# Optimization experiments

Hardware: AMD Instinct MI355X
Metric: run time of the kernel (lower is better)

Reference implementation:

```python
import jax, jax.numpy as jnp
import numpy as np

B, V, E = 32, 2048, 12288
IMG_F = 512
GCN_DIMS = [(3 + IMG_F, 512), (512, 512), (512, 512), (512, 512), (512, 64), (64, 3)]
FC_DIMS = [(V * 3, 1024), (1024, 1024), (1024, V * 3)]


def setup_inputs() -> dict:
    key = jax.random.key(0)
    ks = jax.random.split(key, 3 + len(GCN_DIMS) + len(FC_DIMS))
    inp = {}
    inp["vertices"] = jax.random.normal(ks[0], (B, V, 3), dtype=jnp.float32)
    inp["img_features"] = jax.random.normal(ks[1], (B, IMG_F), dtype=jnp.float32)
    inp["edge_index"] = jax.random.randint(ks[2], (2, E), 0, V, dtype=jnp.int32)
    for i, (fi, fo) in enumerate(GCN_DIMS):
        inp[f"W{i+1}"] = (jax.random.normal(ks[3 + i], (fi, fo), dtype=jnp.float32) / np.sqrt(fi)).astype(jnp.float32)
        inp[f"b{i+1}"] = jnp.zeros((fo,), dtype=jnp.float32)
    for i, (fi, fo) in enumerate(FC_DIMS):
        inp[f"fcW{i+1}"] = (jax.random.normal(ks[3 + len(GCN_DIMS) + i], (fi, fo), dtype=jnp.float32) / np.sqrt(fi)).astype(jnp.float32)
        inp[f"fcb{i+1}"] = jnp.zeros((fo,), dtype=jnp.float32)
    return inp


def _gcn_norm(edge_index):
    # PyG GCNConv: add self-loops, symmetric normalization 1/sqrt(d_i d_j).
    loop = jnp.arange(V, dtype=edge_index.dtype)
    src = jnp.concatenate([edge_index[0], loop])
    dst = jnp.concatenate([edge_index[1], loop])
    deg = jax.ops.segment_sum(jnp.ones_like(dst, dtype=jnp.float32), dst, num_segments=V)
    dinv = jax.lax.rsqrt(deg)  # deg >= 1 due to self-loops
    norm = dinv[src] * dinv[dst]  # [E+V]
    return src, dst, norm


def _gcn_layer(x, W, b, src, dst, norm):
    # x: [B, V, Fin] -> [B, V, Fout]; transform then gather/scatter aggregate.
    h = jnp.einsum("bvi,io->bvo", x, W)
    msg = h[:, src, :] * norm[None, :, None]          # gather over edges
    agg = jax.vmap(lambda m: jax.ops.segment_sum(m, dst, num_segments=V))(msg)
    return agg + b


def reference(vertices, img_features, edge_index,
              W1, b1, W2, b2, W3, b3, W4, b4, W5, b5, W6, b6,
              fcW1, fcb1, fcW2, fcb2, fcW3, fcb3):
    src, dst, norm = _gcn_norm(edge_index)
    # concat vertex coords with broadcast image feature: [B, V, 3+512]
    x = jnp.concatenate([vertices, jnp.broadcast_to(img_features[:, None, :], (B, V, IMG_F))], axis=2)
    x = _gcn_layer(x, W1, b1, src, dst, norm)
    x = _gcn_layer(x, W2, b2, src, dst, norm)
    x = jax.nn.relu(x)
    x = _gcn_layer(x, W3, b3, src, dst, norm)
    x = _gcn_layer(x, W4, b4, src, dst, norm)
    x = jax.nn.relu(x)
    x = _gcn_layer(x, W5, b5, src, dst, norm)
    x = _gcn_layer(x, W6, b6, src, dst, norm)
    x = jax.nn.relu(x)
    x = x.reshape(B, V * 3)
    h = x @ fcW1 + fcb1
    h = h @ fcW2 + fcb2
    h = jnp.tanh(h @ fcW3 + fcb3)
    deformations = h.reshape(B, V, 3) * 0.1
    return vertices + deformations
```

## Files before the change

### kernel.cpp

```cpp
#include <hip/hip_runtime.h>
#include <stdint.h>
#include <math.h>

#define B_ 32
#define V_ 2048
#define E_ 12288
#define M_ (B_*V_)

typedef __bf16 bf16x8 __attribute__((ext_vector_type(8)));
typedef float f32x4 __attribute__((ext_vector_type(4)));

__device__ __forceinline__ float bf2f(unsigned short u){
  union { unsigned int i; float f; } v; v.i = ((unsigned int)u) << 16; return v.f;
}
__device__ __forceinline__ unsigned short f2bf(float f){
  union { float f; unsigned int i; } v; v.f = f;
  unsigned int r = (v.i + 0x7fffu + ((v.i >> 16) & 1u)) >> 16;
  return (unsigned short)r;
}
__device__ __forceinline__ void gload16(const unsigned short* g, unsigned short* l){
  __builtin_amdgcn_global_load_lds(
      (const __attribute__((address_space(1))) void*)g,
      (__attribute__((address_space(3))) void*)l, 16, 0, 0);
}

__global__ __launch_bounds__(1024) void k_pre0(
    const int* __restrict__ ei, int* __restrict__ rowptr_g, int* __restrict__ cols_g,
    float* __restrict__ vals_g, float* __restrict__ selfw_g,
    float* __restrict__ wsum_g, float* __restrict__ w2_g,
    const float* __restrict__ W3, const float* __restrict__ W4,
    const float* __restrict__ img, const float* __restrict__ W1,
    const float* __restrict__ b3, const float* __restrict__ W5,
    const float* __restrict__ W6, const float* __restrict__ b5,
    unsigned short* __restrict__ W3B, unsigned short* __restrict__ W4T,
    float* __restrict__ partB,
    float* __restrict__ C34, float* __restrict__ W56, float* __restrict__ C56){
  __shared__ int   sdeg[V_];
  __shared__ int   srp[V_ + 1];
  __shared__ int   sfill[V_];
  __shared__ float sdinv[V_];
  __shared__ float swsum[V_];
  __shared__ float sw2[V_];
  __shared__ int   swt[16];
  __shared__ __align__(16) float tile[4][32][33];
  if (blockIdx.x == 0){
    const int t = threadIdx.x;
    sdeg[2*t] = 0; sdeg[2*t+1] = 0; sfill[2*t] = 0; sfill[2*t+1] = 0;
    __syncthreads();
    #pragma unroll
    for (int e = t; e < E_; e += 1024) atomicAdd(&sdeg[ei[E_ + e]], 1);
    __syncthreads();
    int c0 = sdeg[2*t], c1 = sdeg[2*t+1];
    int s2 = c0 + c1;
    int lane = t & 63, wid = t >> 6;
    int pre = s2;
    #pragma unroll
    for (int off = 1; off < 64; off <<= 1){
      int u = __shfl_up(pre, off);
      if (lane >= off) pre += u;
    }
    if (lane == 63) swt[wid] = pre;
    __syncthreads();
    if (t == 0){
      int run = 0;
      #pragma unroll
      for (int i = 0; i < 16; i++){ int x = swt[i]; swt[i] = run; run += x; }
      srp[V_] = run;
    }
    __syncthreads();
    int base = swt[wid] + (pre - s2);
    srp[2*t] = base; srp[2*t+1] = base + c0;
    #pragma unroll
    for (int v = t; v < V_; v += 1024){
      float d = (float)(sdeg[v] + 1);
      float di = rsqrtf(d);
      sdinv[v] = di;
      swsum[v] = di * di;
    }
    __syncthreads();
    #pragma unroll
    for (int e = t; e < E_; e += 1024){
      int s = ei[e], d = ei[E_ + e];
      int pos = srp[d] + atomicAdd(&sfill[d], 1);
      float val = sdinv[s] * sdinv[d];
      cols_g[pos] = s;
      vals_g[pos] = val;
      atomicAdd(&swsum[d], val);
    }
    __syncthreads();
    #pragma unroll
    for (int v = t; v < V_; v += 1024)
      sw2[v] = (sdinv[v] * sdinv[v]) * swsum[v];
    __syncthreads();
    #pragma unroll
    for (int e = t; e < E_; e += 1024){
      int s = ei[e], d = ei[E_ + e];
      atomicAdd(&sw2[d], sdinv[s] * sdinv[d] * swsum[s]);
    }
    __syncthreads();
    #pragma unroll
    for (int v = t; v < V_; v += 1024){
      rowptr_g[v] = srp[v];
      selfw_g[v]  = sdinv[v] * sdinv[v];
      wsum_g[v]   = swsum[v];
      w2_g[v]     = sw2[v];
    }
    if (t == 0) rowptr_g[V_] = srp[V_];
  } else {
    int u = blockIdx.x - 1;
    int t10 = threadIdx.x;
    int sub = (u << 2) + (t10 >> 8);
    int t = t10 & 255;
    int ti = t10 >> 8;
    if (sub < 256){
      int tr0 = (sub >> 4) << 5, tc0 = (sub & 15) << 5;
      int r = t >> 5, c = t & 31;
      #pragma unroll
      for (int i = 0; i < 4; i++)
        tile[ti][r + 8*i][c] = W4[(size_t)(tr0 + r + 8*i) * 512 + tc0 + c];
      __syncthreads();
      #pragma unroll
      for (int i = 0; i < 4; i++)
        W4T[(size_t)(tc0 + r + 8*i) * 512 + tr0 + c] = f2bf(tile[ti][c][r + 8*i]);
    } else if (sub < 256 + 1024){
      int id = (sub - 256) * 256 + t;
      W3B[id] = f2bf(W3[id]);
    } else if (sub < 1344){
      int g = sub - 1280;
      int kc = g >> 1, nh = g & 1;
      int k0 = kc * 16;
      float* xs = &tile[ti][0][0];
      for (int i = t; i < 512; i += 256)
        xs[i] = img[(size_t)(i >> 4) * 512 + k0 + (i & 15)];
      __syncthreads();
      const float* W = W1 + 3 * 512;
      int n = (nh << 8) + t;
      float acc[32] = {};
      #pragma unroll
      for (int kg = 0; kg < 4; kg++){
        const float* wp = W + (size_t)(k0 + kg * 4) * 512 + n;
        float w0 = wp[0], w1 = wp[512], w2 = wp[1024], w3 = wp[1536];
        #pragma unroll
        for (int r = 0; r < 32; r++){
          f32x4 xv = *(const f32x4*)&xs[r * 16 + kg * 4];
          acc[r] += xv[0]*w0 + xv[1]*w1 + xv[2]*w2 + xv[3]*w3;
        }
      }
      float* p = partB + (size_t)kc * 16384 + n;
      #pragma unroll
      for (int r = 0; r < 32; r++) p[(size_t)r * 512] = acc[r];
    } else if (sub < 1346){
      int id = (sub - 1344) * 256 + t;
      float a0=0,a1=0,a2=0,a3=0;
      for (int k = 0; k < 512; k += 4){
        a0 += b3[k]   * W4[(size_t)k * 512 + id];
        a1 += b3[k+1] * W4[(size_t)(k+1) * 512 + id];
        a2 += b3[k+2] * W4[(size_t)(k+2) * 512 + id];
        a3 += b3[k+3] * W4[(size_t)(k+3) * 512 + id];
      }
      C34[id] = a0+a1+a2+a3;
    } else if (sub < 1352){
      int i = (sub - 1346) * 256 + t;
      int k5 = i / 3, j = i % 3;
      float a = 0.f;
      #pragma unroll 4
      for (int uu = 0; uu < 64; uu++) a += W5[k5 * 64 + uu] * W6[uu * 3 + j];
      W56[i] = a;
    } else if (sub == 1352){
      if (t < 3){
        float a = 0.f;
        #pragma unroll 4
        for (int uu = 0; uu < 64; uu++) a += b5[uu] * W6[uu * 3 + t];
        C56[t] = a;
      }
    }
  }
}

__global__ __launch_bounds__(256) void k_preC(
    const float* __restrict__ b1, const float* __restrict__ W1,
    const float* __restrict__ W2,
    const float* __restrict__ partIn, float* __restrict__ partOut){
  __shared__ __align__(16) float xs[36 * 16];
  int g = blockIdx.x;
  int kc = g >> 1, k0 = kc * 16;
  int t = threadIdx.x;
  int n = ((g & 1) << 8) + t;
  for (int i = t; i < 576; i += 256){
    int r = i >> 4, kk = i & 15;
    float val;
    if (r == 0)      val = b1[k0 + kk];
    else if (r < 4)  val = W1[(size_t)(r - 1) * 512 + k0 + kk];
    else {
      float a = 0.f;
      #pragma unroll
      for (int s = 0; s < 32; s++)
        a += partIn[(size_t)s * 16384 + (size_t)(r - 4) * 512 + k0 + kk];
      val = a;
    }
    xs[i] = val;
  }
  __syncthreads();
  float acc[36] = {};
  #pragma unroll
  for (int kg = 0; kg < 4; kg++){
    const float* wp = W2 + (size_t)(k0 + kg * 4) * 512 + n;
    float w0 = wp[0], w1 = wp[512], w2 = wp[1024], w3 = wp[1536];
    #pragma unroll
    for (int r = 0; r < 36; r++){
      f32x4 xv = *(const f32x4*)&xs[r * 16 + kg * 4];
      acc[r] += xv[0]*w0 + xv[1]*w1 + xv[2]*w2 + xv[3]*w3;
    }
  }
  float* p = partOut + (size_t)kc * 18432 + n;
  #pragma unroll
  for (int r = 0; r < 36; r++) p[(size_t)r * 512] = acc[r];
}

__global__ __launch_bounds__(256) void k_preD(
    const float* __restrict__ partB, float* __restrict__ P){
  int id = blockIdx.x * 256 + threadIdx.x;
  float a = 0.f;
  #pragma unroll
  for (int s = 0; s < 32; s++) a += partB[(size_t)s * 18432 + id];
  P[id] = a;
}

__global__ __launch_bounds__(256) void k_va2a(
    const float* __restrict__ in, const int* __restrict__ rowptr,
    const int* __restrict__ cols, const float* __restrict__ vals,
    const float* __restrict__ selfw, float* __restrict__ yout){
  __shared__ float xs[V_ * 3];
  int b = blockIdx.y, t = threadIdx.x;
  const float* ib = in + (size_t)b * V_ * 3;
  for (int i = t; i < V_ * 3; i += 256) xs[i] = ib[i];
  __syncthreads();
  int v = blockIdx.x * 256 + t;
  float sw = selfw[v];
  float a0 = sw * xs[v*3], a1 = sw * xs[v*3+1], a2 = sw * xs[v*3+2];
  int re = rowptr[v + 1];
  for (int e = rowptr[v]; e < re; e++){
    int s = cols[e]; float vv = vals[e];
    a0 += vv * xs[s*3]; a1 += vv * xs[s*3+1]; a2 += vv * xs[s*3+2];
  }
  float* o = yout + (size_t)b * V_ * 3 + v * 3;
  o[0] = a0; o[1] = a1; o[2] = a2;
}

__global__ __launch_bounds__(256) void k_va2b(
    const float* __restrict__ yin, const int* __restrict__ rowptr,
    const int* __restrict__ cols, const float* __restrict__ vals,
    const float* __restrict__ selfw, float* __restrict__ outv){
  __shared__ float xs[V_ * 3];
  int b = blockIdx.y, t = threadIdx.x;
  const float* ib = yin + (size_t)b * V_ * 3;
  for (int i = t; i < V_ * 3; i += 256) xs[i] = ib[i];
  __syncthreads();
  int v = blockIdx.x * 256 + t;
  float sw = selfw[v];
  float a0 = sw * xs[v*3], a1 = sw * xs[v*3+1], a2 = sw * xs[v*3+2];
  int re = rowptr[v + 1];
  for (int e = rowptr[v]; e < re; e++){
    int s = cols[e]; float vv = vals[e];
    a0 += vv * xs[s*3]; a1 += vv * xs[s*3+1]; a2 += vv * xs[s*3+2];
  }
  float* o = outv + ((size_t)v * 32 + b) * 3;
  o[0] = a0; o[1] = a1; o[2] = a2;
}

__global__ __launch_bounds__(1024) void k_x2(
    const float* __restrict__ va2v, const float* __restrict__ P,
    const float* __restrict__ wsum, const float* __restrict__ w2s,
    const float* __restrict__ b2,
    unsigned short* __restrict__ Y){
  int v = (blockIdx.x << 2) + (threadIdx.x >> 8);
  int batch = (blockIdx.y << 2) + ((threadIdx.x >> 6) & 3);
  int f8 = (threadIdx.x & 63) * 8;
  const float* va = va2v + ((size_t)v * 32 + batch) * 3;
  float x0 = va[0], x1 = va[1], x2 = va[2];
  float w2v = w2s[v], wsv = wsum[v];
  float tt[8];
  #pragma unroll
  for (int h = 0; h < 2; h++){
    f32x4 wv0 = *(const f32x4*)&P[512  + f8 + 4*h];
    f32x4 wv1 = *(const f32x4*)&P[1024 + f8 + 4*h];
    f32x4 wv2 = *(const f32x4*)&P[1536 + f8 + 4*h];
    f32x4 ccv = *(const f32x4*)&P[f8 + 4*h];
    f32x4 bbv = *(const f32x4*)&b2[f8 + 4*h];
    f32x4 iiv = *(const f32x4*)&P[2048 + (size_t)batch * 512 + f8 + 4*h];
    #pragma unroll
    for (int j = 0; j < 4; j++){
      float tv = x0*wv0[j] + x1*wv1[j] + x2*wv2[j] + w2v*iiv[j] + wsv*ccv[j] + bbv[j];
      tt[4*h + j] = fmaxf(tv, 0.f);
    }
  }
  unsigned int o[4];
  #pragma unroll
  for (int i = 0; i < 4; i++)
    o[i] = (unsigned int)f2bf(tt[2*i]) | ((unsigned int)f2bf(tt[2*i+1]) << 16);
  *(uint4*)&Y[((size_t)v * 32 + batch) * 512 + f8] = *(uint4*)o;
}

__global__ __launch_bounds__(128) void k_aggv(
    const unsigned short* __restrict__ Hg, const int* __restrict__ rowptr,
    const int* __restrict__ cols, const float* __restrict__ vals,
    const float* __restrict__ selfw, unsigned short* __restrict__ Xo){
  int bid = blockIdx.x;
  int bg  = bid & 7;
  int dst = (bid >> 3) & (V_ - 1);
  int fc  = bid >> 14;
  int t = threadIdx.x;
  int batch = (bg << 2) + (t >> 5);
  int f8 = (fc << 8) + (t & 31) * 8;
  int rs = rowptr[dst], re = rowptr[dst + 1];
  float sw = selfw[dst];
  float a[8];
  {
    uint4 q = *(const uint4*)&Hg[((size_t)dst * 32 + batch) * 512 + f8];
    const unsigned int* w = (const unsigned int*)&q;
    #pragma unroll
    for (int i = 0; i < 4; i++){
      a[2*i]   = sw * bf2f(w[i] & 0xffff);
      a[2*i+1] = sw * bf2f(w[i] >> 16);
    }
  }
  int e = rs;
  for (; e + 1 < re; e += 2){
    int s0 = cols[e], s1 = cols[e+1];
    float v0 = vals[e], v1 = vals[e+1];
    uint4 q0 = *(const uint4*)&Hg[((size_t)s0 * 32 + batch) * 512 + f8];
    uint4 q1 = *(const uint4*)&Hg[((size_t)s1 * 32 + batch) * 512 + f8];
    const unsigned int* w0 = (const unsigned int*)&q0;
    const unsigned int* w1 = (const unsigned int*)&q1;
    #pragma unroll
    for (int i = 0; i < 4; i++){
      a[2*i]   += v0 * bf2f(w0[i] & 0xffff) + v1 * bf2f(w1[i] & 0xffff);
      a[2*i+1] += v0 * bf2f(w0[i] >> 16)    + v1 * bf2f(w1[i] >> 16);
    }
  }
  if (e < re){
    int s = cols[e]; float v = vals[e];
    uint4 q = *(const uint4*)&Hg[((size_t)s * 32 + batch) * 512 + f8];
    const unsigned int* w = (const unsigned int*)&q;
    #pragma unroll
    for (int i = 0; i < 4; i++){
      a[2*i]   += v * bf2f(w[i] & 0xffff);
      a[2*i+1] += v * bf2f(w[i] >> 16);
    }
  }
  unsigned int o[4];
  #pragma unroll
  for (int i = 0; i < 4; i++)
    o[i] = (unsigned int)f2bf(a[2*i]) | ((unsigned int)f2bf(a[2*i+1]) << 16);
  *(uint4*)&Xo[((size_t)dst * 32 + batch) * 512 + f8] = *(uint4*)o;
}

template<int BM, int BN, int WM, int WN, int TM, int TN>
__global__ __launch_bounds__(WM*WN*64) void k_gemm(
    const unsigned short* __restrict__ Xg, const unsigned short* __restrict__ Wt,
    unsigned short* __restrict__ Hg, int K, int N,
    const float* __restrict__ wsumv, const float* __restrict__ cvec,
    const float* __restrict__ bias, int relu,
    const float* __restrict__ W56g, float* __restrict__ h5p){
  constexpr int BK = 32;
  constexpr int NW = WM * WN;
  constexpr int NT = NW * 64;
  constexpr int RA = BM / NW;
  constexpr int RB = BN / NW;
  __shared__ __align__(16) unsigned short As[2][BM * BK];
  __shared__ __align__(16) unsigned short Bs[2][BN * BK];
  __shared__ float h5s[BM * 3];
  const int tid = threadIdx.x;
  const int row0 = blockIdx.x * BM, col0 = blockIdx.y * BN;
  const int wave = tid >> 6, lane = tid & 63;
  const int wr = wave / WN, wc = wave % WN;
  const int lrow = lane & 15, lq = lane >> 4;
  const int lrw = lane >> 2, lcol = (lane & 3) * 8;
  const int arow = wave * RA, brow = wave * RB;
  if (h5p){
    for (int i = tid; i < BM * 3; i += NT) h5s[i] = 0.f;
  }
  f32x4 acc[TM][TN] = {};
  #pragma unroll
  for (int t = 0; t < RA / 16; t++)
    gload16(&Xg[(size_t)(row0 + arow + t * 16 + lrw) * K + lcol],
            &As[0][(arow + t * 16) * BK]);
  #pragma unroll
  for (int t = 0; t < RB / 16; t++)
    gload16(&Wt[(size_t)(col0 + brow + t * 16 + lrw) * K + lcol],
            &Bs[0][(brow + t * 16) * BK]);
  int cur = 0;
  for (int k0 = 0; k0 < K; k0 += BK){
    __syncthreads();
    if (k0 + BK < K){
      #pragma unroll
      for (int t = 0; t < RA / 16; t++)
        gload16(&Xg[(size_t)(row0 + arow + t * 16 + lrw) * K + k0 + BK + lcol],
                &As[cur ^ 1][(arow + t * 16) * BK]);
      #pragma unroll
      for (int t = 0; t < RB / 16; t++)
        gload16(&Wt[(size_t)(col0 + brow + t * 16 + lrw) * K + k0 + BK + lcol],
                &Bs[cur ^ 1][(brow + t * 16) * BK]);
    }
    bf16x8 af[TM], bfr[TN];
    #pragma unroll
    for (int tm = 0; tm < TM; tm++)
      af[tm] = *(const bf16x8*)&As[cur][(wr * TM * 16 + tm * 16 + lrow) * BK + lq * 8];
    #pragma unroll
    for (int tn = 0; tn < TN; tn++)
      bfr[tn] = *(const bf16x8*)&Bs[cur][(wc * TN * 16 + tn * 16 + lrow) * BK + lq * 8];
    #pragma unroll
    for (int tm = 0; tm < TM; tm++)
      #pragma unroll
      for (int tn = 0; tn < TN; tn++)
        acc[tm][tn] = __builtin_amdgcn_mfma_f32_16x16x32_bf16(af[tm], bfr[tn], acc[tm][tn], 0, 0, 0);
    cur ^= 1;
  }
  if (h5p){
    float w56l[TN][3], cvl[TN], bvl[TN];
    #pragma unroll
    for (int tn = 0; tn < TN; tn++){
      int col = col0 + wc * TN * 16 + tn * 16 + lrow;
      cvl[tn] = cvec[col]; bvl[tn] = bias[col];
      w56l[tn][0] = W56g[col * 3];
      w56l[tn][1] = W56g[col * 3 + 1];
      w56l[tn][2] = W56g[col * 3 + 2];
    }
    #pragma unroll
    for (int tm = 0; tm < TM; tm++){
      #pragma unroll
      for (int r = 0; r < 4; r++){
        int lr = wr * TM * 16 + tm * 16 + lq * 4 + r;
        float ws = wsumv[(row0 + lr) >> 5];
        float p0 = 0.f, p1 = 0.f, p2 = 0.f;
        #pragma unroll
        for (int tn = 0; tn < TN; tn++){
          float x = fmaxf(acc[tm][tn][r] + ws * cvl[tn] + bvl[tn], 0.f);
          p0 += x * w56l[tn][0]; p1 += x * w56l[tn][1]; p2 += x * w56l[tn][2];
        }
        #pragma unroll
        for (int off = 8; off; off >>= 1){
          p0 += __shfl_down(p0, off);
          p1 += __shfl_down(p1, off);
          p2 += __shfl_down(p2, off);
        }
        if (lrow == 0){
          atomicAdd(&h5s[lr * 3 + 0], p0);
          atomicAdd(&h5s[lr * 3 + 1], p1);
          atomicAdd(&h5s[lr * 3 + 2], p2);
        }
      }
    }
    __syncthreads();
    float* dst = h5p + (size_t)blockIdx.y * ((size_t)M_ * 3) + (size_t)row0 * 3;
    for (int i = tid; i < BM * 3; i += NT) dst[i] = h5s[i];
  } else {
    #pragma unroll
    for (int tm = 0; tm < TM; tm++){
      #pragma unroll
      for (int tn = 0; tn < TN; tn++){
        int col = col0 + wc * TN * 16 + tn * 16 + lrow;
        float cv = 0.f, bv = 0.f;
        if (cvec){ cv = cvec[col]; bv = bias[col]; }
        #pragma unroll
        for (int r = 0; r < 4; r++){
          int row = row0 + wr * TM * 16 + tm * 16 + lq * 4 + r;
          float x = acc[tm][tn][r];
          if (cvec) x += wsumv[row >> 5] * cv + bv;
          if (relu) x = fmaxf(x, 0.f);
          Hg[(size_t)row * N + col] = f2bf(x);
        }
      }
    }
  }
}

__global__ __launch_bounds__(256) void k_xa2a(
    const float* __restrict__ h5p, const int* __restrict__ rowptr,
    const int* __restrict__ cols, const float* __restrict__ vals,
    const float* __restrict__ selfw, float* __restrict__ yout){
  __shared__ float xs[V_ * 3];
  int b = blockIdx.y, t = threadIdx.x;
  const size_t M3 = (size_t)M_ * 3;
  for (int i = t; i < V_ * 3; i += 256){
    int v = i / 3, j = i - v * 3;
    size_t g = ((size_t)v * 32 + b) * 3 + j;
    xs[i] = h5p[g] + h5p[M3 + g] + h5p[2 * M3 + g] + h5p[3 * M3 + g];
  }
  __syncthreads();
  int v = blockIdx.x * 256 + t;
  float sw = selfw[v];
  float a0 = sw * xs[v*3], a1 = sw * xs[v*3+1], a2 = sw * xs[v*3+2];
  int re = rowptr[v + 1];
  for (int e = rowptr[v]; e < re; e++){
    int s = cols[e]; float vv = vals[e];
    a0 += vv * xs[s*3]; a1 += vv * xs[s*3+1]; a2 += vv * xs[s*3+2];
  }
  float* o = yout + (size_t)b * V_ * 3 + v * 3;
  o[0] = a0; o[1] = a1; o[2] = a2;
}

__global__ __launch_bounds__(256) void k_xa2b(
    const float* __restrict__ yin, const int* __restrict__ rowptr,
    const int* __restrict__ cols, const float* __restrict__ vals,
    const float* __restrict__ selfw, const float* __restrict__ wsum,
    const float* __restrict__ C56, const float* __restrict__ b6,
    float* __restrict__ XF){
  __shared__ float xs[V_ * 3];
  int b = blockIdx.y, t = threadIdx.x;
  const float* ib = yin + (size_t)b * V_ * 3;
  for (int i = t; i < V_ * 3; i += 256) xs[i] = ib[i];
  __syncthreads();
  int v = blockIdx.x * 256 + t;
  float sw = selfw[v];
  float a0 = sw * xs[v*3], a1 = sw * xs[v*3+1], a2 = sw * xs[v*3+2];
  int re = rowptr[v + 1];
  for (int e = rowptr[v]; e < re; e++){
    int s = cols[e]; float vv = vals[e];
    a0 += vv * xs[s*3]; a1 += vv * xs[s*3+1]; a2 += vv * xs[s*3+2];
  }
  float w = wsum[v];
  a0 = fmaxf(a0 + w * C56[0] + b6[0], 0.f);
  a1 = fmaxf(a1 + w * C56[1] + b6[1], 0.f);
  a2 = fmaxf(a2 + w * C56[2] + b6[2], 0.f);
  float* ob = XF + (size_t)b * V_ * 3 + v * 3;
  ob[0] = a0; ob[1] = a1; ob[2] = a2;
}

template<int R, int KC>
__global__ __launch_bounds__(256) void k_fcp(
    const float* __restrict__ in, const float* __restrict__ W,
    float* __restrict__ partial, int K, int N){
  const int n = blockIdx.x * 256 + threadIdx.x;
  const int k0 = blockIdx.y * KC;
  float acc[R] = {};
  for (int kk = 0; kk < KC; kk += 4){
    const float* wp = W + (size_t)(k0 + kk) * N + n;
    float w0 = wp[0];
    float w1 = wp[(size_t)N];
    float w2 = wp[(size_t)2 * N];
    float w3 = wp[(size_t)3 * N];
    #pragma unroll
    for (int r = 0; r < R; r++){
      const float* xp = in + (size_t)r * K + k0 + kk;
      acc[r] += xp[0]*w0 + xp[1]*w1 + xp[2]*w2 + xp[3]*w3;
    }
  }
  float* p = partial + (size_t)blockIdx.y * R * N + n;
  #pragma unroll
  for (int r = 0; r < R; r++) p[(size_t)r * N] = acc[r];
}

__global__ __launch_bounds__(256) void k_fcr(
    const float* __restrict__ partial, const float* __restrict__ bias,
    float* __restrict__ out, int total, int N, int KS, int mode,
    const float* __restrict__ vert){
  int id = blockIdx.x * 256 + threadIdx.x;
  if (id >= total) return;
  int n = id % N;
  float a0 = 0.f, a1 = 0.f, a2 = 0.f, a3 = 0.f;
  int s = 0;
  for (; s + 4 <= KS; s += 4){
    a0 += partial[(size_t)s * total + id];
    a1 += partial[(size_t)(s + 1) * total + id];
    a2 += partial[(size_t)(s + 2) * total + id];
    a3 += partial[(size_t)(s + 3) * total + id];
  }
  for (; s < KS; s++) a0 += partial[(size_t)s * total + id];
  float acc = a0 + a1 + a2 + a3;
  if (bias) acc += bias[n];
  if (mode) acc = vert[id] + 0.1f * tanhf(acc);
  out[id] = acc;
}

static constexpr size_t AL(size_t x){ return (x + 255) & ~(size_t)255; }
static constexpr size_t S512 = (size_t)M_ * 512 * 2;
static constexpr size_t S3   = (size_t)M_ * 3 * 4;
static constexpr size_t OXA  = 0;
static constexpr size_t OXB  = OXA  + AL(S512);
static constexpr size_t OVA2 = OXB  + AL(S512);
static constexpr size_t OH5P = OVA2 + AL(S3);
static constexpr size_t OXF  = OH5P + AL(4 * S3);
static constexpr size_t OFC1 = OXF  + AL(S3);
static constexpr size_t OFC2 = OFC1 + AL((size_t)B_ * 1024 * 4);
static constexpr size_t OI1  = OFC2 + AL((size_t)B_ * 1024 * 4);
static constexpr size_t OP   = OI1  + AL((size_t)32 * 512 * 4);
static constexpr size_t OC34 = OP   + AL((size_t)36 * 512 * 4);
static constexpr size_t OW56 = OC34 + AL((size_t)512 * 4);
static constexpr size_t OC56 = OW56 + AL((size_t)512 * 3 * 4);
static constexpr size_t OW3B = OC56 + AL((size_t)3 * 4);
static constexpr size_t OW4T = OW3B + AL((size_t)512 * 512 * 2);
static constexpr size_t OW34 = OW4T + AL((size_t)512 * 512 * 2);
static constexpr size_t OROW = OW34 + AL((size_t)512 * 512 * 2);
static constexpr size_t OCOL = OROW + AL((size_t)(V_ + 1) * 4);
static constexpr size_t OVAL = OCOL + AL((size_t)E_ * 4);
static constexpr size_t OSELF= OVAL + AL((size_t)E_ * 4);
static constexpr size_t OWS  = OSELF+ AL((size_t)V_ * 4);
static constexpr size_t OW2S = OWS  + AL((size_t)V_ * 4);

extern "C" void kernel_launch(void* const* d_in, const int* in_sizes, int n_in,
                              void* d_out, int out_size, void* d_ws, size_t ws_size,
                              hipStream_t stream){
  const float* vert  = (const float*)d_in[0];
  const float* img   = (const float*)d_in[1];
  const int*   ei    = (const int*)  d_in[2];
  const float* W1 = (const float*)d_in[3],  *b1 = (const float*)d_in[4];
  const float* W2 = (const float*)d_in[5],  *b2 = (const float*)d_in[6];
  const float* W3 = (const float*)d_in[7],  *b3 = (const float*)d_in[8];
  const float* W4 = (const float*)d_in[9],  *b4 = (const float*)d_in[10];
  const float* W5 = (const float*)d_in[11], *b5 = (const float*)d_in[12];
  const float* W6 = (const float*)d_in[13], *b6 = (const float*)d_in[14];
  const float* fcW1 = (const float*)d_in[15], *fcb1 = (const float*)d_in[16];
  const float* fcW2 = (const float*)d_in[17], *fcb2 = (const float*)d_in[18];
  const float* fcW3 = (const float*)d_in[19], *fcb3 = (const float*)d_in[20];
  float* out = (float*)d_out;

  char* ws = (char*)d_ws;
  unsigned short* XA  = (unsigned short*)(ws + OXA);
  unsigned short* XB  = (unsigned short*)(ws + OXB);
  float* VA2v = (float*)(ws + OVA2);
  float* H5P  = (float*)(ws + OH5P);
  float* XF   = (float*)(ws + OXF);
  float* FC1o = (float*)(ws + OFC1);
  float* FC2o = (float*)(ws + OFC2);
  float* P    = (float*)(ws + OP);
  float* C34  = (float*)(ws + OC34);
  float* W56  = (float*)(ws + OW56);
  float* C56  = (float*)(ws + OC56);
  unsigned short* W3B = (unsigned short*)(ws + OW3B);
  unsigned short* W4T = (unsigned short*)(ws + OW4T);
  unsigned short* W34 = (unsigned short*)(ws + OW34);
  float* PARTA = (float*)(ws + OXA);
  float* PARTB = (float*)(ws + OXB);
  float* PARTC = (float*)(ws + OXB) + (1 << 20);
  float* YTMP  = (float*)(ws + OXA);
  int*   ROW  = (int*)(ws + OROW);
  int*   COL  = (int*)(ws + OCOL);
  float* VAL  = (float*)(ws + OVAL);
  float* SELF = (float*)(ws + OSELF);
  float* WSUM = (float*)(ws + OWS);
  float* W2S  = (float*)(ws + OW2S);

  k_pre0<<<340, 1024, 0, stream>>>(ei, ROW, COL, VAL, SELF, WSUM, W2S,
                                   W3, W4, img, W1, b3, W5, W6, b5,
                                   W3B, W4T, PARTB, C34, W56, C56);
  k_preC<<<64, 256, 0, stream>>>(b1, W1, W2, PARTB, PARTC);
  k_preD<<<72, 256, 0, stream>>>(PARTC, P);
  k_gemm<64,64,2,2,2,2><<<dim3(8, 8), 256, 0, stream>>>(W4T, W3B, W34, 512, 512,
                                                        nullptr, nullptr, nullptr, 0,
                                                        nullptr, nullptr);

  k_va2a<<<dim3(8, B_), 256, 0, stream>>>(vert, ROW, COL, VAL, SELF, YTMP);
  k_va2b<<<dim3(8, B_), 256, 0, stream>>>(YTMP, ROW, COL, VAL, SELF, VA2v);
  k_x2<<<dim3(V_ / 4, 8), 1024, 0, stream>>>(VA2v, P, WSUM, W2S, b2, XA);
  k_aggv<<<V_ * 16, 128, 0, stream>>>(XA, ROW, COL, VAL, SELF, XB);
  k_aggv<<<V_ * 16, 128, 0, stream>>>(XB, ROW, COL, VAL, SELF, XA);

  k_gemm<128,128,2,2,4,4><<<dim3(M_ / 128, 4), 256, 0, stream>>>(XA, W34, XB, 512, 512,
                                                                 WSUM, C34, b4, 1,
                                                                 W56, H5P);

  k_xa2a<<<dim3(8, B_), 256, 0, stream>>>(H5P, ROW, COL, VAL, SELF, YTMP);
  k_xa2b<<<dim3(8, B_), 256, 0, stream>>>(YTMP, ROW, COL, VAL, SELF, WSUM, C56, b6, XF);

  k_fcp<32,64><<<dim3(4, 96), 256, 0, stream>>>(XF, fcW1, PARTA, 6144, 1024);
  k_fcr<<<(B_ * 1024 + 255) / 256, 256, 0, stream>>>(PARTA, fcb1, FC1o, 32 * 1024, 1024, 96, 0, nullptr);
  k_fcp<32,64><<<dim3(4, 16), 256, 0, stream>>>(FC1o, fcW2, PARTA, 1024, 1024);
  k_fcr<<<(B_ * 1024 + 255) / 256, 256, 0, stream>>>(PARTA, fcb2, FC2o, 32 * 1024, 1024, 16, 0, nullptr);
  k_fcp<32,64><<<dim3(24, 16), 256, 0, stream>>>(FC2o, fcW3, PARTA, 1024, 6144);
  k_fcr<<<(B_ * 6144 + 255) / 256, 256, 0, stream>>>(PARTA, fcb3, out, 32 * 6144, 6144, 16, 1, vert);
}
```

Measured before the change: 498.2 us.

## Merge independent precompute kernels and fuse x2 construction into first aggregation

```diff
diff --git a/kernel.cpp b/kernel.cpp
--- a/kernel.cpp
+++ b/kernel.cpp
@@ -177,186 +177,9 @@
   }
 }
 
-__global__ __launch_bounds__(256) void k_preC(
-    const float* __restrict__ b1, const float* __restrict__ W1,
-    const float* __restrict__ W2,
-    const float* __restrict__ partIn, float* __restrict__ partOut){
-  __shared__ __align__(16) float xs[36 * 16];
-  int g = blockIdx.x;
-  int kc = g >> 1, k0 = kc * 16;
-  int t = threadIdx.x;
-  int n = ((g & 1) << 8) + t;
-  for (int i = t; i < 576; i += 256){
-    int r = i >> 4, kk = i & 15;
-    float val;
-    if (r == 0)      val = b1[k0 + kk];
-    else if (r < 4)  val = W1[(size_t)(r - 1) * 512 + k0 + kk];
-    else {
-      float a = 0.f;
-      #pragma unroll
-      for (int s = 0; s < 32; s++)
-        a += partIn[(size_t)s * 16384 + (size_t)(r - 4) * 512 + k0 + kk];
-      val = a;
-    }
-    xs[i] = val;
-  }
-  __syncthreads();
-  float acc[36] = {};
-  #pragma unroll
-  for (int kg = 0; kg < 4; kg++){
-    const float* wp = W2 + (size_t)(k0 + kg * 4) * 512 + n;
-    float w0 = wp[0], w1 = wp[512], w2 = wp[1024], w3 = wp[1536];
-    #pragma unroll
-    for (int r = 0; r < 36; r++){
-      f32x4 xv = *(const f32x4*)&xs[r * 16 + kg * 4];
-      acc[r] += xv[0]*w0 + xv[1]*w1 + xv[2]*w2 + xv[3]*w3;
-    }
-  }
-  float* p = partOut + (size_t)kc * 18432 + n;
-  #pragma unroll
-  for (int r = 0; r < 36; r++) p[(size_t)r * 512] = acc[r];
-}
-
-__global__ __launch_bounds__(256) void k_preD(
-    const float* __restrict__ partB, float* __restrict__ P){
-  int id = blockIdx.x * 256 + threadIdx.x;
-  float a = 0.f;
-  #pragma unroll
-  for (int s = 0; s < 32; s++) a += partB[(size_t)s * 18432 + id];
-  P[id] = a;
-}
-
-__global__ __launch_bounds__(256) void k_va2a(
-    const float* __restrict__ in, const int* __restrict__ rowptr,
-    const int* __restrict__ cols, const float* __restrict__ vals,
-    const float* __restrict__ selfw, float* __restrict__ yout){
-  __shared__ float xs[V_ * 3];
-  int b = blockIdx.y, t = threadIdx.x;
-  const float* ib = in + (size_t)b * V_ * 3;
-  for (int i = t; i < V_ * 3; i += 256) xs[i] = ib[i];
-  __syncthreads();
-  int v = blockIdx.x * 256 + t;
-  float sw = selfw[v];
-  float a0 = sw * xs[v*3], a1 = sw * xs[v*3+1], a2 = sw * xs[v*3+2];
-  int re = rowptr[v + 1];
-  for (int e = rowptr[v]; e < re; e++){
-    int s = cols[e]; float vv = vals[e];
-    a0 += vv * xs[s*3]; a1 += vv * xs[s*3+1]; a2 += vv * xs[s*3+2];
-  }
-  float* o = yout + (size_t)b * V_ * 3 + v * 3;
-  o[0] = a0; o[1] = a1; o[2] = a2;
-}
-
-__global__ __launch_bounds__(256) void k_va2b(
-    const float* __restrict__ yin, const int* __restrict__ rowptr,
-    const int* __restrict__ cols, const float* __restrict__ vals,
-    const float* __restrict__ selfw, float* __restrict__ outv){
-  __shared__ float xs[V_ * 3];
-  int b = blockIdx.y, t = threadIdx.x;
-  const float* ib = yin + (size_t)b * V_ * 3;
-  for (int i = t; i < V_ * 3; i += 256) xs[i] = ib[i];
-  __syncthreads();
-  int v = blockIdx.x * 256 + t;
-  float sw = selfw[v];
-  float a0 = sw * xs[v*3], a1 = sw * xs[v*3+1], a2 = sw * xs[v*3+2];
-  int re = rowptr[v + 1];
-  for (int e = rowptr[v]; e < re; e++){
-    int s = cols[e]; float vv = vals[e];
-    a0 += vv * xs[s*3]; a1 += vv * xs[s*3+1]; a2 += vv * xs[s*3+2];
-  }
-  float* o = outv + ((size_t)v * 32 + b) * 3;
-  o[0] = a0; o[1] = a1; o[2] = a2;
-}
-
-__global__ __launch_bounds__(1024) void k_x2(
-    const float* __restrict__ va2v, const float* __restrict__ P,
-    const float* __restrict__ wsum, const float* __restrict__ w2s,
-    const float* __restrict__ b2,
-    unsigned short* __restrict__ Y){
-  int v = (blockIdx.x << 2) + (threadIdx.x >> 8);
-  int batch = (blockIdx.y << 2) + ((threadIdx.x >> 6) & 3);
-  int f8 = (threadIdx.x & 63) * 8;
-  const float* va = va2v + ((size_t)v * 32 + batch) * 3;
-  float x0 = va[0], x1 = va[1], x2 = va[2];
-  float w2v = w2s[v], wsv = wsum[v];
-  float tt[8];
-  #pragma unroll
-  for (int h = 0; h < 2; h++){
-    f32x4 wv0 = *(const f32x4*)&P[512  + f8 + 4*h];
-    f32x4 wv1 = *(const f32x4*)&P[1024 + f8 + 4*h];
-    f32x4 wv2 = *(const f32x4*)&P[1536 + f8 + 4*h];
-    f32x4 ccv = *(const f32x4*)&P[f8 + 4*h];
-    f32x4 bbv = *(const f32x4*)&b2[f8 + 4*h];
-    f32x4 iiv = *(const f32x4*)&P[2048 + (size_t)batch * 512 + f8 + 4*h];
-    #pragma unroll
-    for (int j = 0; j < 4; j++){
-      float tv = x0*wv0[j] + x1*wv1[j] + x2*wv2[j] + w2v*iiv[j] + wsv*ccv[j] + bbv[j];
-      tt[4*h + j] = fmaxf(tv, 0.f);
-    }
-  }
-  unsigned int o[4];
-  #pragma unroll
-  for (int i = 0; i < 4; i++)
-    o[i] = (unsigned int)f2bf(tt[2*i]) | ((unsigned int)f2bf(tt[2*i+1]) << 16);
-  *(uint4*)&Y[((size_t)v * 32 + batch) * 512 + f8] = *(uint4*)o;
-}
-
-__global__ __launch_bounds__(128) void k_aggv(
-    const unsigned short* __restrict__ Hg, const int* __restrict__ rowptr,
-    const int* __restrict__ cols, const float* __restrict__ vals,
-    const float* __restrict__ selfw, unsigned short* __restrict__ Xo){
-  int bid = blockIdx.x;
-  int bg  = bid & 7;
-  int dst = (bid >> 3) & (V_ - 1);
-  int fc  = bid >> 14;
-  int t = threadIdx.x;
-  int batch = (bg << 2) + (t >> 5);
-  int f8 = (fc << 8) + (t & 31) * 8;
-  int rs = rowptr[dst], re = rowptr[dst + 1];
-  float sw = selfw[dst];
-  float a[8];
-  {
-    uint4 q = *(const uint4*)&Hg[((size_t)dst * 32 + batch) * 512 + f8];
-    const unsigned int* w = (const unsigned int*)&q;
-    #pragma unroll
-    for (int i = 0; i < 4; i++){
-      a[2*i]   = sw * bf2f(w[i] & 0xffff);
-      a[2*i+1] = sw * bf2f(w[i] >> 16);
-    }
-  }
-  int e = rs;
-  for (; e + 1 < re; e += 2){
-    int s0 = cols[e], s1 = cols[e+1];
-    float v0 = vals[e], v1 = vals[e+1];
-    uint4 q0 = *(const uint4*)&Hg[((size_t)s0 * 32 + batch) * 512 + f8];
-    uint4 q1 = *(const uint4*)&Hg[((size_t)s1 * 32 + batch) * 512 + f8];
-    const unsigned int* w0 = (const unsigned int*)&q0;
-    const unsigned int* w1 = (const unsigned int*)&q1;
-    #pragma unroll
-    for (int i = 0; i < 4; i++){
-      a[2*i]   += v0 * bf2f(w0[i] & 0xffff) + v1 * bf2f(w1[i] & 0xffff);
-      a[2*i+1] += v0 * bf2f(w0[i] >> 16)    + v1 * bf2f(w1[i] >> 16);
-    }
-  }
-  if (e < re){
-    int s = cols[e]; float v = vals[e];
-    uint4 q = *(const uint4*)&Hg[((size_t)s * 32 + batch) * 512 + f8];
-    const unsigned int* w = (const unsigned int*)&q;
-    #pragma unroll
-    for (int i = 0; i < 4; i++){
-      a[2*i]   += v * bf2f(w[i] & 0xffff);
-      a[2*i+1] += v * bf2f(w[i] >> 16);
-    }
-  }
-  unsigned int o[4];
-  #pragma unroll
-  for (int i = 0; i < 4; i++)
-    o[i] = (unsigned int)f2bf(a[2*i]) | ((unsigned int)f2bf(a[2*i+1]) << 16);
-  *(uint4*)&Xo[((size_t)dst * 32 + batch) * 512 + f8] = *(uint4*)o;
-}
-
 template<int BM, int BN, int WM, int WN, int TM, int TN>
-__global__ __launch_bounds__(WM*WN*64) void k_gemm(
+__device__ __forceinline__ void gemm_body(
+    int bx, int by,
     const unsigned short* __restrict__ Xg, const unsigned short* __restrict__ Wt,
     unsigned short* __restrict__ Hg, int K, int N,
     const float* __restrict__ wsumv, const float* __restrict__ cvec,
@@ -371,7 +194,7 @@
   __shared__ __align__(16) unsigned short Bs[2][BN * BK];
   __shared__ float h5s[BM * 3];
   const int tid = threadIdx.x;
-  const int row0 = blockIdx.x * BM, col0 = blockIdx.y * BN;
+  const int row0 = bx * BM, col0 = by * BN;
   const int wave = tid >> 6, lane = tid & 63;
   const int wr = wave / WN, wc = wave % WN;
   const int lrow = lane & 15, lq = lane >> 4;
@@ -452,7 +275,7 @@
       }
     }
     __syncthreads();
-    float* dst = h5p + (size_t)blockIdx.y * ((size_t)M_ * 3) + (size_t)row0 * 3;
+    float* dst = h5p + (size_t)by * ((size_t)M_ * 3) + (size_t)row0 * 3;
     for (int i = tid; i < BM * 3; i += NT) dst[i] = h5s[i];
   } else {
     #pragma unroll
@@ -473,6 +296,212 @@
       }
     }
   }
+}
+
+template<int BM, int BN, int WM, int WN, int TM, int TN>
+__global__ __launch_bounds__(WM*WN*64) void k_gemm(
+    const unsigned short* __restrict__ Xg, const unsigned short* __restrict__ Wt,
+    unsigned short* __restrict__ Hg, int K, int N,
+    const float* __restrict__ wsumv, const float* __restrict__ cvec,
+    const float* __restrict__ bias, int relu,
+    const float* __restrict__ W56g, float* __restrict__ h5p){
+  gemm_body<BM,BN,WM,WN,TM,TN>(blockIdx.x, blockIdx.y, Xg, Wt, Hg, K, N,
+                               wsumv, cvec, bias, relu, W56g, h5p);
+}
+
+__device__ __forceinline__ void preC_body(
+    int g, const float* __restrict__ b1, const float* __restrict__ W1,
+    const float* __restrict__ W2,
+    const float* __restrict__ partIn, float* __restrict__ partOut){
+  __shared__ __align__(16) float xs[36 * 16];
+  int kc = g >> 1, k0 = kc * 16;
+  int t = threadIdx.x;
+  int n = ((g & 1) << 8) + t;
+  for (int i = t; i < 576; i += 256){
+    int r = i >> 4, kk = i & 15;
+    float val;
+    if (r == 0)      val = b1[k0 + kk];
+    else if (r < 4)  val = W1[(size_t)(r - 1) * 512 + k0 + kk];
+    else {
+      float a = 0.f;
+      #pragma unroll
+      for (int s = 0; s < 32; s++)
+        a += partIn[(size_t)s * 16384 + (size_t)(r - 4) * 512 + k0 + kk];
+      val = a;
+    }
+    xs[i] = val;
+  }
+  __syncthreads();
+  float acc[36] = {};
+  #pragma unroll
+  for (int kg = 0; kg < 4; kg++){
+    const float* wp = W2 + (size_t)(k0 + kg * 4) * 512 + n;
+    float w0 = wp[0], w1 = wp[512], w2 = wp[1024], w3 = wp[1536];
+    #pragma unroll
+    for (int r = 0; r < 36; r++){
+      f32x4 xv = *(const f32x4*)&xs[r * 16 + kg * 4];
+      acc[r] += xv[0]*w0 + xv[1]*w1 + xv[2]*w2 + xv[3]*w3;
+    }
+  }
+  float* p = partOut + (size_t)kc * 18432 + n;
+  #pragma unroll
+  for (int r = 0; r < 36; r++) p[(size_t)r * 512] = acc[r];
+}
+
+__device__ __forceinline__ void va2_body(
+    int bx, int b, const float* __restrict__ in, const int* __restrict__ rowptr,
+    const int* __restrict__ cols, const float* __restrict__ vals,
+    const float* __restrict__ selfw, float* __restrict__ outp, int out_vmajor){
+  __shared__ float xs[V_ * 3];
+  int t = threadIdx.x;
+  const float* ib = in + (size_t)b * V_ * 3;
+  for (int i = t; i < V_ * 3; i += 256) xs[i] = ib[i];
+  __syncthreads();
+  int v = bx * 256 + t;
+  float sw = selfw[v];
+  float a0 = sw * xs[v*3], a1 = sw * xs[v*3+1], a2 = sw * xs[v*3+2];
+  int re = rowptr[v + 1];
+  for (int e = rowptr[v]; e < re; e++){
+    int s = cols[e]; float vv = vals[e];
+    a0 += vv * xs[s*3]; a1 += vv * xs[s*3+1]; a2 += vv * xs[s*3+2];
+  }
+  float* o = out_vmajor ? (outp + ((size_t)v * 32 + b) * 3)
+                        : (outp + (size_t)b * V_ * 3 + (size_t)v * 3);
+  o[0] = a0; o[1] = a1; o[2] = a2;
+}
+
+__global__ __launch_bounds__(256) void k_mix1(
+    const unsigned short* __restrict__ W4T, const unsigned short* __restrict__ W3B,
+    unsigned short* __restrict__ W34,
+    const float* __restrict__ b1, const float* __restrict__ W1,
+    const float* __restrict__ W2,
+    const float* __restrict__ partIn, float* __restrict__ partOut,
+    const float* __restrict__ vert, const int* __restrict__ rowptr,
+    const int* __restrict__ cols, const float* __restrict__ vals,
+    const float* __restrict__ selfw, float* __restrict__ ytmp){
+  int blk = blockIdx.x;
+  if (blk < 64){
+    gemm_body<64,64,2,2,2,2>(blk & 7, blk >> 3, W4T, W3B, W34, 512, 512,
+                             nullptr, nullptr, nullptr, 0, nullptr, nullptr);
+  } else if (blk < 128){
+    preC_body(blk - 64, b1, W1, W2, partIn, partOut);
+  } else {
+    int r = blk - 128;
+    va2_body(r & 7, r >> 3, vert, rowptr, cols, vals, selfw, ytmp, 0);
+  }
+}
+
+__global__ __launch_bounds__(256) void k_mix2(
+    const float* __restrict__ partC, float* __restrict__ P,
+    const float* __restrict__ ytmp, const int* __restrict__ rowptr,
+    const int* __restrict__ cols, const float* __restrict__ vals,
+    const float* __restrict__ selfw, float* __restrict__ va2v){
+  int blk = blockIdx.x;
+  if (blk < 72){
+    int id = blk * 256 + threadIdx.x;
+    float a = 0.f;
+    #pragma unroll
+    for (int s = 0; s < 32; s++) a += partC[(size_t)s * 18432 + id];
+    P[id] = a;
+  } else {
+    int r = blk - 72;
+    va2_body(r & 7, r >> 3, ytmp, rowptr, cols, vals, selfw, va2v, 1);
+  }
+}
+
+__global__ __launch_bounds__(256) void k_y1(
+    const float* __restrict__ va2v, const float* __restrict__ P,
+    const float* __restrict__ wsum, const float* __restrict__ w2s,
+    const float* __restrict__ b2,
+    const int* __restrict__ rowptr, const int* __restrict__ cols,
+    const float* __restrict__ vals, const float* __restrict__ selfw,
+    unsigned short* __restrict__ Y){
+  int dst = blockIdx.x;
+  int batch = (blockIdx.y << 2) + (threadIdx.x >> 6);
+  int f8 = (threadIdx.x & 63) * 8;
+  float wv0[8], wv1[8], wv2[8], cc[8], bb[8], ii[8];
+  #pragma unroll
+  for (int j = 0; j < 8; j++){
+    int fc = f8 + j;
+    wv0[j] = P[512 + fc]; wv1[j] = P[1024 + fc]; wv2[j] = P[1536 + fc];
+    cc[j]  = P[fc];       bb[j]  = b2[fc];
+    ii[j]  = P[2048 + (size_t)batch * 512 + fc];
+  }
+  float acc[8] = {};
+  int rs = rowptr[dst], re = rowptr[dst + 1];
+  for (int e = rs - 1; e < re; e++){
+    int s; float w;
+    if (e < rs){ s = dst; w = selfw[dst]; }
+    else       { s = cols[e]; w = vals[e]; }
+    const float* va = va2v + ((size_t)s * 32 + batch) * 3;
+    float x0 = va[0], x1 = va[1], x2 = va[2];
+    float w2v = w2s[s], wsv = wsum[s];
+    #pragma unroll
+    for (int j = 0; j < 8; j++){
+      float tv = x0*wv0[j] + x1*wv1[j] + x2*wv2[j] + w2v*ii[j] + wsv*cc[j] + bb[j];
+      tv = fmaxf(tv, 0.f);
+      acc[j] += w * tv;
+    }
+  }
+  unsigned int o[4];
+  #pragma unroll
+  for (int i = 0; i < 4; i++)
+    o[i] = (unsigned int)f2bf(acc[2*i]) | ((unsigned int)f2bf(acc[2*i+1]) << 16);
+  *(uint4*)&Y[((size_t)dst * 32 + batch) * 512 + f8] = *(uint4*)o;
+}
+
+__global__ __launch_bounds__(128) void k_aggv(
+    const unsigned short* __restrict__ Hg, const int* __restrict__ rowptr,
+    const int* __restrict__ cols, const float* __restrict__ vals,
+    const float* __restrict__ selfw, unsigned short* __restrict__ Xo){
+  int bid = blockIdx.x;
+  int bg  = bid & 7;
+  int dst = (bid >> 3) & (V_ - 1);
+  int fc  = bid >> 14;
+  int t = threadIdx.x;
+  int batch = (bg << 2) + (t >> 5);
+  int f8 = (fc << 8) + (t & 31) * 8;
+  int rs = rowptr[dst], re = rowptr[dst + 1];
+  float sw = selfw[dst];
+  float a[8];
+  {
+    uint4 q = *(const uint4*)&Hg[((size_t)dst * 32 + batch) * 512 + f8];
+    const unsigned int* w = (const unsigned int*)&q;
+    #pragma unroll
+    for (int i = 0; i < 4; i++){
+      a[2*i]   = sw * bf2f(w[i] & 0xffff);
+      a[2*i+1] = sw * bf2f(w[i] >> 16);
+    }
+  }
+  int e = rs;
+  for (; e + 1 < re; e += 2){
+    int s0 = cols[e], s1 = cols[e+1];
+    float v0 = vals[e], v1 = vals[e+1];
+    uint4 q0 = *(const uint4*)&Hg[((size_t)s0 * 32 + batch) * 512 + f8];
+    uint4 q1 = *(const uint4*)&Hg[((size_t)s1 * 32 + batch) * 512 + f8];
+    const unsigned int* w0 = (const unsigned int*)&q0;
+    const unsigned int* w1 = (const unsigned int*)&q1;
+    #pragma unroll
+    for (int i = 0; i < 4; i++){
+      a[2*i]   += v0 * bf2f(w0[i] & 0xffff) + v1 * bf2f(w1[i] & 0xffff);
+      a[2*i+1] += v0 * bf2f(w0[i] >> 16)    + v1 * bf2f(w1[i] >> 16);
+    }
+  }
+  if (e < re){
+    int s = cols[e]; float v = vals[e];
+    uint4 q = *(const uint4*)&Hg[((size_t)s * 32 + batch) * 512 + f8];
+    const unsigned int* w = (const unsigned int*)&q;
+    #pragma unroll
+    for (int i = 0; i < 4; i++){
+      a[2*i]   += v * bf2f(w[i] & 0xffff);
+      a[2*i+1] += v * bf2f(w[i] >> 16);
+    }
+  }
+  unsigned int o[4];
+  #pragma unroll
+  for (int i = 0; i < 4; i++)
+    o[i] = (unsigned int)f2bf(a[2*i]) | ((unsigned int)f2bf(a[2*i+1]) << 16);
+  *(uint4*)&Xo[((size_t)dst * 32 + batch) * 512 + f8] = *(uint4*)o;
 }
 
 __global__ __launch_bounds__(256) void k_xa2a(
@@ -644,16 +673,12 @@
   k_pre0<<<340, 1024, 0, stream>>>(ei, ROW, COL, VAL, SELF, WSUM, W2S,
                                    W3, W4, img, W1, b3, W5, W6, b5,
                                    W3B, W4T, PARTB, C34, W56, C56);
-  k_preC<<<64, 256, 0, stream>>>(b1, W1, W2, PARTB, PARTC);
-  k_preD<<<72, 256, 0, stream>>>(PARTC, P);
-  k_gemm<64,64,2,2,2,2><<<dim3(8, 8), 256, 0, stream>>>(W4T, W3B, W34, 512, 512,
-                                                        nullptr, nullptr, nullptr, 0,
-                                                        nullptr, nullptr);
-
-  k_va2a<<<dim3(8, B_), 256, 0, stream>>>(vert, ROW, COL, VAL, SELF, YTMP);
-  k_va2b<<<dim3(8, B_), 256, 0, stream>>>(YTMP, ROW, COL, VAL, SELF, VA2v);
-  k_x2<<<dim3(V_ / 4, 8), 1024, 0, stream>>>(VA2v, P, WSUM, W2S, b2, XA);
-  k_aggv<<<V_ * 16, 128, 0, stream>>>(XA, ROW, COL, VAL, SELF, XB);
+
+  k_mix1<<<384, 256, 0, stream>>>(W4T, W3B, W34, b1, W1, W2, PARTB, PARTC,
+                                  vert, ROW, COL, VAL, SELF, YTMP);
+  k_mix2<<<328, 256, 0, stream>>>(PARTC, P, YTMP, ROW, COL, VAL, SELF, VA2v);
+
+  k_y1<<<dim3(V_, 8), 256, 0, stream>>>(VA2v, P, WSUM, W2S, b2, ROW, COL, VAL, SELF, XB);
   k_aggv<<<V_ * 16, 128, 0, stream>>>(XB, ROW, COL, VAL, SELF, XA);
 
   k_gemm<128,128,2,2,4,4><<<dim3(M_ / 128, 4), 256, 0, stream>>>(XA, W34, XB, 512, 512,
```

New measurement: 493.2 us. About the same (-1.0%).
